# Kernel tuning notes

Measured on AMD Instinct MI355X. Metric: run time of the kernel, lower is better.

The kernel has to match this reference:

```python
import jax, jax.numpy as jnp
import numpy as np

N_NODES = 100000
N_EDGES = 3200000
F_IN = 128
F_OUT = 32
N_GRAPHS = 64


def setup_inputs() -> dict:
    key = jax.random.key(0)
    ks = jax.random.split(key, 12)
    x = jax.random.normal(ks[0], (N_NODES, F_IN), dtype=jnp.float32)
    edge_attr = jax.random.normal(ks[1], (N_EDGES, 1), dtype=jnp.float32)
    edge_index = jax.random.randint(ks[2], (2, N_EDGES), 0, N_NODES, dtype=jnp.int64)
    batch = jnp.sort(jax.random.randint(ks[3], (N_NODES,), 0, N_GRAPHS, dtype=jnp.int64))
    s = 1.0 / np.sqrt(F_IN)
    W_l = jax.random.normal(ks[4], (F_IN, F_OUT), dtype=jnp.float32) * s
    b_l = jnp.zeros((F_OUT,), dtype=jnp.float32)
    W_r = jax.random.normal(ks[5], (F_IN, F_OUT), dtype=jnp.float32) * s
    b_r = jnp.zeros((F_OUT,), dtype=jnp.float32)
    W_e = jax.random.normal(ks[6], (1, F_OUT), dtype=jnp.float32)
    att = jax.random.normal(ks[7], (F_OUT,), dtype=jnp.float32) * (1.0 / np.sqrt(F_OUT))
    bias = jnp.zeros((F_OUT,), dtype=jnp.float32)
    return {"x": x, "edge_attr": edge_attr, "W_l": W_l, "b_l": b_l,
            "W_r": W_r, "b_r": b_r, "W_e": W_e, "att": att, "bias": bias,
            "edge_index": edge_index, "batch": batch}


def reference(x, edge_attr, W_l, b_l, W_r, b_r, W_e, att, bias, edge_index, batch):
    # GATv2Conv (heads=1, concat=True, edge_dim=1, negative_slope=0.2)
    src = edge_index[0]  # message source j
    dst = edge_index[1]  # message target i
    xl = x @ W_l + b_l            # [N, F_OUT] source transform
    xr = x @ W_r + b_r            # [N, F_OUT] target transform
    e = edge_attr @ W_e           # [E, F_OUT] edge feature embedding
    m = xl[src] + xr[dst] + e     # [E, F_OUT]
    m = jax.nn.leaky_relu(m, negative_slope=0.2)
    logit = m @ att               # [E] per-edge attention logit
    # segment softmax over incoming edges of each target node
    mx = jax.ops.segment_max(logit, dst, num_segments=N_NODES)
    alpha = jnp.exp(logit - mx[dst])
    denom = jax.ops.segment_sum(alpha, dst, num_segments=N_NODES)
    alpha = alpha / (denom[dst] + 1e-16)
    # weighted scatter aggregation of source messages, then output bias
    out = jax.ops.segment_sum(xl[src] * alpha[:, None], dst, num_segments=N_NODES) + bias
    # global_mean_pool over graphs
    cnt = jax.ops.segment_sum(jnp.ones((N_NODES,), x.dtype), batch, num_segments=N_GRAPHS)
    pooled = jax.ops.segment_sum(out, batch, num_segments=N_GRAPHS) / jnp.maximum(cnt, 1.0)[:, None]
    return pooled  # [N_GRAPHS, F_OUT]
```

## Files before the change

kernel.cpp:

```cpp
#include <hip/hip_runtime.h>

#define N_NODES 100000
#define N_EDGES 3200000
#define F_IN 128
#define F_OUT 32
#define N_GRAPHS 64

__global__ __launch_bounds__(256) void gat_transform(
    const float* __restrict__ x,
    const float* __restrict__ Wl, const float* __restrict__ bl,
    const float* __restrict__ Wr, const float* __restrict__ br,
    float* __restrict__ xl, float* __restrict__ xr)
{
    __shared__ float sWl[F_IN * F_OUT];
    __shared__ float sWr[F_IN * F_OUT];
    for (int i = threadIdx.x; i < F_IN * F_OUT; i += 256) {
        sWl[i] = Wl[i];
        sWr[i] = Wr[i];
    }
    __syncthreads();

    const int f     = threadIdx.x & 31;
    const int local = threadIdx.x >> 5;
    const int node  = blockIdx.x * 8 + local;
    if (node >= N_NODES) return;

    const float4* xrow = (const float4*)(x + (size_t)node * F_IN);
    float accl = bl[f];
    float accr = br[f];
#pragma unroll
    for (int k4 = 0; k4 < F_IN / 4; ++k4) {
        float4 v = xrow[k4];
        const int k = k4 * 4;
        accl += v.x * sWl[(k + 0) * 32 + f];  accr += v.x * sWr[(k + 0) * 32 + f];
        accl += v.y * sWl[(k + 1) * 32 + f];  accr += v.y * sWr[(k + 1) * 32 + f];
        accl += v.z * sWl[(k + 2) * 32 + f];  accr += v.z * sWr[(k + 2) * 32 + f];
        accl += v.w * sWl[(k + 3) * 32 + f];  accr += v.w * sWr[(k + 3) * 32 + f];
    }
    xl[(size_t)node * 32 + f] = accl;
    xr[(size_t)node * 32 + f] = accr;
}

__global__ __launch_bounds__(256) void gat_edge(
    const int* __restrict__ ei,
    const float* __restrict__ eattr,
    const float* __restrict__ We,
    const float* __restrict__ att,
    const float* __restrict__ xl, const float* __restrict__ xr,
    float* __restrict__ outacc,
    float* __restrict__ denom)
{
    const int f = threadIdx.x & 31;
    const float attf = att[f];
    const float wef  = We[f];

    const int group   = (blockIdx.x * blockDim.x + threadIdx.x) >> 5;
    const int ngroups = (gridDim.x * blockDim.x) >> 5;

    for (int e = group; e < N_EDGES; e += ngroups) {
        const int src = ei[e];
        const int dst = ei[N_EDGES + e];
        const float ea = eattr[e];

        const float xlv = xl[(size_t)src * 32 + f];
        float m = xlv + xr[(size_t)dst * 32 + f] + ea * wef;
        m = (m > 0.f) ? m : 0.2f * m;

        float t = m * attf;
        t += __shfl_xor(t, 16, 32);
        t += __shfl_xor(t, 8, 32);
        t += __shfl_xor(t, 4, 32);
        t += __shfl_xor(t, 2, 32);
        t += __shfl_xor(t, 1, 32);

        const float p = __expf(t);
        atomicAdd(&outacc[(size_t)dst * 32 + f], xlv * p);
        if (f == 0) atomicAdd(&denom[dst], p);
    }
}

__global__ __launch_bounds__(256) void gat_pool(
    const float* __restrict__ outacc, const float* __restrict__ denom,
    const float* __restrict__ bias, const int* __restrict__ batch,
    float* __restrict__ out)
{
    const int g = blockIdx.x;
    __shared__ int s_lo, s_hi;
    if (threadIdx.x == 0) {
        int lo = 0, hi = N_NODES;
        while (lo < hi) { int mid = (lo + hi) >> 1; if (batch[mid] < g) lo = mid + 1; else hi = mid; }
        s_lo = lo;
        lo = 0; hi = N_NODES;
        while (lo < hi) { int mid = (lo + hi) >> 1; if (batch[mid] < g + 1) lo = mid + 1; else hi = mid; }
        s_hi = lo;
    }
    __syncthreads();
    const int lo = s_lo, hi = s_hi;

    const int f   = threadIdx.x & 31;
    const int grp = threadIdx.x >> 5;

    float acc = 0.f;
    for (int n = lo + grp; n < hi; n += 8) {
        const float d = denom[n];
        acc += outacc[(size_t)n * 32 + f] / (d + 1e-16f);
    }

    __shared__ float s_acc[8][32];
    s_acc[grp][f] = acc;
    __syncthreads();

    if (threadIdx.x < 32) {
        float sum = 0.f;
#pragma unroll
        for (int i = 0; i < 8; ++i) sum += s_acc[i][f];
        const int cnt = hi - lo;
        out[g * 32 + f] = (cnt > 0) ? (sum / (float)cnt + bias[f]) : 0.f;
    }
}

extern "C" void kernel_launch(void* const* d_in, const int* in_sizes, int n_in,
                              void* d_out, int out_size, void* d_ws, size_t ws_size,
                              hipStream_t stream)
{
    const float* x     = (const float*)d_in[0];
    const float* eattr = (const float*)d_in[1];
    const float* Wl    = (const float*)d_in[2];
    const float* bl    = (const float*)d_in[3];
    const float* Wr    = (const float*)d_in[4];
    const float* br    = (const float*)d_in[5];
    const float* We    = (const float*)d_in[6];
    const float* att   = (const float*)d_in[7];
    const float* bias  = (const float*)d_in[8];
    const int*   ei    = (const int*)d_in[9];
    const int*   batch = (const int*)d_in[10];
    float* out = (float*)d_out;

    float* ws = (float*)d_ws;
    float* xl     = ws;
    float* xr     = ws + (size_t)N_NODES * 32;
    float* outacc = ws + (size_t)N_NODES * 64;
    float* denom  = ws + (size_t)N_NODES * 96;

    hipMemsetAsync(outacc, 0, (size_t)N_NODES * 33 * sizeof(float), stream);

    gat_transform<<<(N_NODES + 7) / 8, 256, 0, stream>>>(x, Wl, bl, Wr, br, xl, xr);
    gat_edge<<<4096, 256, 0, stream>>>(ei, eattr, We, att, xl, xr, outacc, denom);
    gat_pool<<<N_GRAPHS, 256, 0, stream>>>(outacc, denom, bias, batch, out);
}
```

Before: 623.9 us.

## Build CSR by destination each call and aggregate per node without atomics

Replaces the per-edge atomic scatter with an on-device CSR build (degree histogram, two-level scan, atomic-offset scatter of src and edge_attr pairs). A per-node wavefront then gathers its incoming edges and keeps accumulator and denominator in registers. The normalized result is written in place over xr, which removes the float atomics into a 100000x32 buffer and the division in the pool kernel. The trade is several extra passes over the edge list plus integer atomics in the histogram and scatter steps, and per-node loops that are imbalanced when degrees vary. If the workspace is too small it falls back to the old atomic path.

```diff
diff --git a/kernel.cpp b/kernel.cpp
--- a/kernel.cpp
+++ b/kernel.cpp
@@ -5,6 +5,9 @@
 #define F_IN 128
 #define F_OUT 32
 #define N_GRAPHS 64
+
+#define SCAN_CHUNK 512
+#define N_CHUNKS ((N_NODES + SCAN_CHUNK - 1) / SCAN_CHUNK)
 
 __global__ __launch_bounds__(256) void gat_transform(
     const float* __restrict__ x,
@@ -41,48 +44,130 @@
     xr[(size_t)node * 32 + f] = accr;
 }
 
-__global__ __launch_bounds__(256) void gat_edge(
-    const int* __restrict__ ei,
-    const float* __restrict__ eattr,
-    const float* __restrict__ We,
-    const float* __restrict__ att,
-    const float* __restrict__ xl, const float* __restrict__ xr,
-    float* __restrict__ outacc,
-    float* __restrict__ denom)
-{
-    const int f = threadIdx.x & 31;
+__global__ __launch_bounds__(256) void csr_hist(const int* __restrict__ ei,
+                                                int* __restrict__ deg)
+{
+    const int stride = gridDim.x * blockDim.x;
+    for (int e = blockIdx.x * blockDim.x + threadIdx.x; e < N_EDGES; e += stride)
+        atomicAdd(&deg[ei[N_EDGES + e]], 1);
+}
+
+__global__ __launch_bounds__(256) void csr_scan_partial(const int* __restrict__ deg,
+                                                        int* __restrict__ partial)
+{
+    __shared__ int s[256];
+    const int c = blockIdx.x;
+    int v = 0;
+#pragma unroll
+    for (int r = 0; r < SCAN_CHUNK / 256; ++r) {
+        const int i = c * SCAN_CHUNK + r * 256 + threadIdx.x;
+        if (i < N_NODES) v += deg[i];
+    }
+    s[threadIdx.x] = v;
+    __syncthreads();
+    for (int off = 128; off > 0; off >>= 1) {
+        if (threadIdx.x < off) s[threadIdx.x] += s[threadIdx.x + off];
+        __syncthreads();
+    }
+    if (threadIdx.x == 0) partial[c] = s[0];
+}
+
+__global__ __launch_bounds__(256) void csr_scan_base(const int* __restrict__ partial,
+                                                     int* __restrict__ cbase)
+{
+    __shared__ int s[256];
+    const int t = threadIdx.x;
+    const int v = (t < N_CHUNKS) ? partial[t] : 0;
+    s[t] = v;
+    __syncthreads();
+    for (int off = 1; off < 256; off <<= 1) {
+        int u = (t >= off) ? s[t - off] : 0;
+        __syncthreads();
+        s[t] += u;
+        __syncthreads();
+    }
+    if (t < N_CHUNKS) cbase[t] = s[t] - v;
+}
+
+__global__ __launch_bounds__(256) void csr_scan_write(const int* __restrict__ deg,
+                                                      const int* __restrict__ cbase,
+                                                      int* __restrict__ rowptr,
+                                                      int* __restrict__ wofs)
+{
+    __shared__ int s[256];
+    const int c = blockIdx.x, t = threadIdx.x;
+    const int i0 = c * SCAN_CHUNK + 2 * t;
+    const int i1 = i0 + 1;
+    const int v0 = (i0 < N_NODES) ? deg[i0] : 0;
+    const int v1 = (i1 < N_NODES) ? deg[i1] : 0;
+    const int pv = v0 + v1;
+    s[t] = pv;
+    __syncthreads();
+    for (int off = 1; off < 256; off <<= 1) {
+        int u = (t >= off) ? s[t - off] : 0;
+        __syncthreads();
+        s[t] += u;
+        __syncthreads();
+    }
+    const int excl = s[t] - pv + cbase[c];
+    if (i0 < N_NODES) { rowptr[i0] = excl;      wofs[i0] = excl; }
+    if (i1 < N_NODES) { rowptr[i1] = excl + v0; wofs[i1] = excl + v0; }
+    if (c == 0 && t == 0) rowptr[N_NODES] = N_EDGES;
+}
+
+__global__ __launch_bounds__(256) void csr_scatter(const int* __restrict__ ei,
+                                                   const float* __restrict__ eattr,
+                                                   int* __restrict__ wofs,
+                                                   int2* __restrict__ es2)
+{
+    const int stride = gridDim.x * blockDim.x;
+    for (int e = blockIdx.x * blockDim.x + threadIdx.x; e < N_EDGES; e += stride) {
+        const int src = ei[e];
+        const int dst = ei[N_EDGES + e];
+        const int pos = atomicAdd(&wofs[dst], 1);
+        es2[pos] = make_int2(src, __float_as_int(eattr[e]));
+    }
+}
+
+__global__ __launch_bounds__(256) void gat_aggregate(
+    const int2* __restrict__ es2, const int* __restrict__ rowptr,
+    const float* __restrict__ We, const float* __restrict__ att,
+    const float* __restrict__ xl, float* xrh)
+{
+    const int f    = threadIdx.x & 31;
+    const int node = blockIdx.x * 8 + (threadIdx.x >> 5);
+    if (node >= N_NODES) return;
+
     const float attf = att[f];
     const float wef  = We[f];
-
-    const int group   = (blockIdx.x * blockDim.x + threadIdx.x) >> 5;
-    const int ngroups = (gridDim.x * blockDim.x) >> 5;
-
-    for (int e = group; e < N_EDGES; e += ngroups) {
-        const int src = ei[e];
-        const int dst = ei[N_EDGES + e];
-        const float ea = eattr[e];
-
+    const float xrf  = xrh[(size_t)node * 32 + f];
+    const int beg = rowptr[node];
+    const int end = rowptr[node + 1];
+
+    float acc = 0.f, den = 0.f;
+    for (int j = beg; j < end; ++j) {
+        const int2 pe = es2[j];
+        const int   src = pe.x;
+        const float ea  = __int_as_float(pe.y);
         const float xlv = xl[(size_t)src * 32 + f];
-        float m = xlv + xr[(size_t)dst * 32 + f] + ea * wef;
+        float m = xlv + xrf + ea * wef;
         m = (m > 0.f) ? m : 0.2f * m;
-
         float t = m * attf;
         t += __shfl_xor(t, 16, 32);
         t += __shfl_xor(t, 8, 32);
         t += __shfl_xor(t, 4, 32);
         t += __shfl_xor(t, 2, 32);
         t += __shfl_xor(t, 1, 32);
-
         const float p = __expf(t);
-        atomicAdd(&outacc[(size_t)dst * 32 + f], xlv * p);
-        if (f == 0) atomicAdd(&denom[dst], p);
-    }
+        acc += xlv * p;
+        den += p;
+    }
+    xrh[(size_t)node * 32 + f] = acc / (den + 1e-16f);
 }
 
 __global__ __launch_bounds__(256) void gat_pool(
-    const float* __restrict__ outacc, const float* __restrict__ denom,
-    const float* __restrict__ bias, const int* __restrict__ batch,
-    float* __restrict__ out)
+    const float* __restrict__ h, const float* __restrict__ bias,
+    const int* __restrict__ batch, float* __restrict__ out)
 {
     const int g = blockIdx.x;
     __shared__ int s_lo, s_hi;
@@ -101,10 +186,8 @@
     const int grp = threadIdx.x >> 5;
 
     float acc = 0.f;
-    for (int n = lo + grp; n < hi; n += 8) {
-        const float d = denom[n];
-        acc += outacc[(size_t)n * 32 + f] / (d + 1e-16f);
-    }
+    for (int n = lo + grp; n < hi; n += 8)
+        acc += h[(size_t)n * 32 + f];
 
     __shared__ float s_acc[8][32];
     s_acc[grp][f] = acc;
@@ -115,7 +198,70 @@
 #pragma unroll
         for (int i = 0; i < 8; ++i) sum += s_acc[i][f];
         const int cnt = hi - lo;
-        out[g * 32 + f] = (cnt > 0) ? (sum / (float)cnt + bias[f]) : 0.f;
+        out[g * 32 + f] = (cnt > 0) ? (sum / (float)cnt + bias[f]) : bias[f];
+    }
+}
+
+__global__ __launch_bounds__(256) void gat_edge_atomic(
+    const int* __restrict__ ei, const float* __restrict__ eattr,
+    const float* __restrict__ We, const float* __restrict__ att,
+    const float* __restrict__ xl, const float* __restrict__ xr,
+    float* __restrict__ outacc, float* __restrict__ denom)
+{
+    const int f = threadIdx.x & 31;
+    const float attf = att[f];
+    const float wef  = We[f];
+    const int group   = (blockIdx.x * blockDim.x + threadIdx.x) >> 5;
+    const int ngroups = (gridDim.x * blockDim.x) >> 5;
+    for (int e = group; e < N_EDGES; e += ngroups) {
+        const int src = ei[e];
+        const int dst = ei[N_EDGES + e];
+        const float xlv = xl[(size_t)src * 32 + f];
+        float m = xlv + xr[(size_t)dst * 32 + f] + eattr[e] * wef;
+        m = (m > 0.f) ? m : 0.2f * m;
+        float t = m * attf;
+        t += __shfl_xor(t, 16, 32);
+        t += __shfl_xor(t, 8, 32);
+        t += __shfl_xor(t, 4, 32);
+        t += __shfl_xor(t, 2, 32);
+        t += __shfl_xor(t, 1, 32);
+        const float p = __expf(t);
+        atomicAdd(&outacc[(size_t)dst * 32 + f], xlv * p);
+        if (f == 0) atomicAdd(&denom[dst], p);
+    }
+}
+
+__global__ __launch_bounds__(256) void gat_pool_div(
+    const float* __restrict__ outacc, const float* __restrict__ denom,
+    const float* __restrict__ bias, const int* __restrict__ batch,
+    float* __restrict__ out)
+{
+    const int g = blockIdx.x;
+    __shared__ int s_lo, s_hi;
+    if (threadIdx.x == 0) {
+        int lo = 0, hi = N_NODES;
+        while (lo < hi) { int mid = (lo + hi) >> 1; if (batch[mid] < g) lo = mid + 1; else hi = mid; }
+        s_lo = lo;
+        lo = 0; hi = N_NODES;
+        while (lo < hi) { int mid = (lo + hi) >> 1; if (batch[mid] < g + 1) lo = mid + 1; else hi = mid; }
+        s_hi = lo;
+    }
+    __syncthreads();
+    const int lo = s_lo, hi = s_hi;
+    const int f   = threadIdx.x & 31;
+    const int grp = threadIdx.x >> 5;
+    float acc = 0.f;
+    for (int n = lo + grp; n < hi; n += 8)
+        acc += outacc[(size_t)n * 32 + f] / (denom[n] + 1e-16f);
+    __shared__ float s_acc[8][32];
+    s_acc[grp][f] = acc;
+    __syncthreads();
+    if (threadIdx.x < 32) {
+        float sum = 0.f;
+#pragma unroll
+        for (int i = 0; i < 8; ++i) sum += s_acc[i][f];
+        const int cnt = hi - lo;
+        out[g * 32 + f] = (cnt > 0) ? (sum / (float)cnt + bias[f]) : bias[f];
     }
 }
 
@@ -137,14 +283,41 @@
     float* out = (float*)d_out;
 
     float* ws = (float*)d_ws;
-    float* xl     = ws;
-    float* xr     = ws + (size_t)N_NODES * 32;
-    float* outacc = ws + (size_t)N_NODES * 64;
-    float* denom  = ws + (size_t)N_NODES * 96;
-
-    hipMemsetAsync(outacc, 0, (size_t)N_NODES * 33 * sizeof(float), stream);
-
-    gat_transform<<<(N_NODES + 7) / 8, 256, 0, stream>>>(x, Wl, bl, Wr, br, xl, xr);
-    gat_edge<<<4096, 256, 0, stream>>>(ei, eattr, We, att, xl, xr, outacc, denom);
-    gat_pool<<<N_GRAPHS, 256, 0, stream>>>(outacc, denom, bias, batch, out);
-}
+    const size_t NF = (size_t)N_NODES * 32;
+
+    const size_t need_csr = (NF * 2) * 4 + (size_t)N_EDGES * 8
+                          + ((size_t)N_NODES * 2 + 1 + 256) * 4;
+
+    if (ws_size >= need_csr) {
+        float* xl  = ws;
+        float* xrh = ws + NF;
+        int2*  es2 = (int2*)(ws + 2 * NF);
+        int*   deg    = (int*)(es2 + N_EDGES);
+        int*   rowptr = deg + N_NODES;
+        int*   wofs   = rowptr + N_NODES + 1;
+        int*   partial = wofs + N_NODES;
+        int*   cbase   = partial;
+        cbase = partial + 256;
+
+        hipMemsetAsync(deg, 0, N_NODES * sizeof(int), stream);
+
+        csr_hist<<<2048, 256, 0, stream>>>(ei, deg);
+        csr_scan_partial<<<N_CHUNKS, 256, 0, stream>>>(deg, partial);
+        csr_scan_base<<<1, 256, 0, stream>>>(partial, cbase);
+        csr_scan_write<<<N_CHUNKS, 256, 0, stream>>>(deg, cbase, rowptr, wofs);
+        csr_scatter<<<2048, 256, 0, stream>>>(ei, eattr, wofs, es2);
+
+        gat_transform<<<(N_NODES + 7) / 8, 256, 0, stream>>>(x, Wl, bl, Wr, br, xl, xrh);
+        gat_aggregate<<<(N_NODES + 7) / 8, 256, 0, stream>>>(es2, rowptr, We, att, xl, xrh);
+        gat_pool<<<N_GRAPHS, 256, 0, stream>>>(xrh, bias, batch, out);
+    } else {
+        float* xl     = ws;
+        float* xr     = ws + NF;
+        float* outacc = ws + 2 * NF;
+        float* denom  = ws + 3 * NF;
+        hipMemsetAsync(outacc, 0, (NF + N_NODES) * sizeof(float), stream);
+        gat_transform<<<(N_NODES + 7) / 8, 256, 0, stream>>>(x, Wl, bl, Wr, br, xl, xr);
+        gat_edge_atomic<<<4096, 256, 0, stream>>>(ei, eattr, We, att, xl, xr, outacc, denom);
+        gat_pool_div<<<N_GRAPHS, 256, 0, stream>>>(outacc, denom, bias, batch, out);
+    }
+}
```

Result: slower. 711.0 us (+14.0%).

## Bucket edges by destination and aggregate per-bucket in shared memory

Applied to the files above, without the earlier changes.

Replaces the global-atomic edge kernel with a counting-sort of edges into destination buckets of 49 nodes (histogram, scan, scatter with packed src/local-dst/attr), then a per-bucket kernel that keeps xr, accumulators and denominators in shared memory and writes normalized outputs. This removes global float atomics on 3.2M×32 features and the separate normalization read in pooling. It adds two extra passes over the edge list plus a scatter with global atomics on counters. Weights are also interleaved as float2 in the transform kernel.

```diff
diff --git a/kernel.cpp b/kernel.cpp
--- a/kernel.cpp
+++ b/kernel.cpp
@@ -6,23 +6,25 @@
 #define F_OUT 32
 #define N_GRAPHS 64
 
+#define NB 2048
+#define BN 49
+#define NSLICE 8
+#define NCNT (NB * NSLICE)
+#define HGRID 2048
+
 __global__ __launch_bounds__(256) void gat_transform(
     const float* __restrict__ x,
     const float* __restrict__ Wl, const float* __restrict__ bl,
     const float* __restrict__ Wr, const float* __restrict__ br,
     float* __restrict__ xl, float* __restrict__ xr)
 {
-    __shared__ float sWl[F_IN * F_OUT];
-    __shared__ float sWr[F_IN * F_OUT];
-    for (int i = threadIdx.x; i < F_IN * F_OUT; i += 256) {
-        sWl[i] = Wl[i];
-        sWr[i] = Wr[i];
-    }
-    __syncthreads();
-
-    const int f     = threadIdx.x & 31;
-    const int local = threadIdx.x >> 5;
-    const int node  = blockIdx.x * 8 + local;
+    __shared__ float2 sW[F_IN * F_OUT];
+    for (int i = threadIdx.x; i < F_IN * F_OUT; i += 256)
+        sW[i] = make_float2(Wl[i], Wr[i]);
+    __syncthreads();
+
+    const int f    = threadIdx.x & 31;
+    const int node = blockIdx.x * 8 + (threadIdx.x >> 5);
     if (node >= N_NODES) return;
 
     const float4* xrow = (const float4*)(x + (size_t)node * F_IN);
@@ -32,57 +34,148 @@
     for (int k4 = 0; k4 < F_IN / 4; ++k4) {
         float4 v = xrow[k4];
         const int k = k4 * 4;
-        accl += v.x * sWl[(k + 0) * 32 + f];  accr += v.x * sWr[(k + 0) * 32 + f];
-        accl += v.y * sWl[(k + 1) * 32 + f];  accr += v.y * sWr[(k + 1) * 32 + f];
-        accl += v.z * sWl[(k + 2) * 32 + f];  accr += v.z * sWr[(k + 2) * 32 + f];
-        accl += v.w * sWl[(k + 3) * 32 + f];  accr += v.w * sWr[(k + 3) * 32 + f];
+        float2 w0 = sW[(k + 0) * 32 + f]; accl += v.x * w0.x; accr += v.x * w0.y;
+        float2 w1 = sW[(k + 1) * 32 + f]; accl += v.y * w1.x; accr += v.y * w1.y;
+        float2 w2 = sW[(k + 2) * 32 + f]; accl += v.z * w2.x; accr += v.z * w2.y;
+        float2 w3 = sW[(k + 3) * 32 + f]; accl += v.w * w3.x; accr += v.w * w3.y;
     }
     xl[(size_t)node * 32 + f] = accl;
     xr[(size_t)node * 32 + f] = accr;
 }
 
-__global__ __launch_bounds__(256) void gat_edge(
-    const int* __restrict__ ei,
-    const float* __restrict__ eattr,
-    const float* __restrict__ We,
-    const float* __restrict__ att,
-    const float* __restrict__ xl, const float* __restrict__ xr,
-    float* __restrict__ outacc,
-    float* __restrict__ denom)
-{
-    const int f = threadIdx.x & 31;
+__global__ __launch_bounds__(256) void bkt_hist(const int* __restrict__ ei,
+                                                int* __restrict__ cnt)
+{
+    const int slice  = blockIdx.x & (NSLICE - 1);
+    const int stride = gridDim.x * blockDim.x;
+    for (int e = blockIdx.x * blockDim.x + threadIdx.x; e < N_EDGES; e += stride) {
+        const int dst = ei[N_EDGES + e];
+        atomicAdd(&cnt[(dst / BN) * NSLICE + slice], 1);
+    }
+}
+
+__global__ __launch_bounds__(256) void bkt_scan(const int* __restrict__ cnt,
+                                                int* __restrict__ base,
+                                                int* __restrict__ cursor)
+{
+    __shared__ int s[256];
+    const int t = threadIdx.x;
+    const int R = NCNT / 256;
+    int sum = 0;
+    for (int r = 0; r < R; ++r) sum += cnt[t * R + r];
+    s[t] = sum;
+    __syncthreads();
+    for (int off = 1; off < 256; off <<= 1) {
+        int u = (t >= off) ? s[t - off] : 0;
+        __syncthreads();
+        s[t] += u;
+        __syncthreads();
+    }
+    int run = s[t] - sum;
+    for (int r = 0; r < R; ++r) {
+        const int i = t * R + r;
+        const int c = cnt[i];
+        base[i] = run;
+        cursor[i] = run;
+        run += c;
+    }
+    if (t == 255) base[NCNT] = run;
+}
+
+__global__ __launch_bounds__(256) void bkt_scatter(const int* __restrict__ ei,
+                                                   const float* __restrict__ eattr,
+                                                   int* __restrict__ cursor,
+                                                   int2* __restrict__ es2)
+{
+    const int slice  = blockIdx.x & (NSLICE - 1);
+    const int stride = gridDim.x * blockDim.x;
+    for (int e = blockIdx.x * blockDim.x + threadIdx.x; e < N_EDGES; e += stride) {
+        const int src = ei[e];
+        const int dst = ei[N_EDGES + e];
+        const int b   = dst / BN;
+        const int dl  = dst - b * BN;
+        const int pos = atomicAdd(&cursor[b * NSLICE + slice], 1);
+        es2[pos] = make_int2(src | (dl << 17), __float_as_int(eattr[e]));
+    }
+}
+
+#define PROCESS(e, xv) do {                                                   \
+    const int dl_ = (e).x >> 17;                                              \
+    float m_ = (xv) + sxr[dl_ * 32 + f] + __int_as_float((e).y) * wef;        \
+    m_ = (m_ > 0.f) ? m_ : 0.2f * m_;                                         \
+    float t_ = m_ * attf;                                                     \
+    t_ += __shfl_xor(t_, 16, 32);                                             \
+    t_ += __shfl_xor(t_, 8, 32);                                              \
+    t_ += __shfl_xor(t_, 4, 32);                                              \
+    t_ += __shfl_xor(t_, 2, 32);                                              \
+    t_ += __shfl_xor(t_, 1, 32);                                              \
+    const float p_ = __expf(t_);                                              \
+    atomicAdd(&sacc[dl_ * 32 + f], (xv) * p_);                                \
+    if (f == 0) atomicAdd(&sden[dl_], p_);                                    \
+} while (0)
+
+__global__ __launch_bounds__(256) void gat_aggregate(
+    const int2* __restrict__ es2, const int* __restrict__ base,
+    const float* __restrict__ We, const float* __restrict__ att,
+    const float* __restrict__ xl, float* xrh)
+{
+    __shared__ float sxr[BN * 32];
+    __shared__ float sacc[BN * 32];
+    __shared__ float sden[BN];
+
+    const int b    = blockIdx.x;
+    const int n0   = b * BN;
+    const int n1   = (n0 + BN < N_NODES) ? (n0 + BN) : N_NODES;
+    const int nrow = n1 - n0;
+    const int tid  = threadIdx.x;
+
+    if (nrow > 0) {
+        for (int i = tid; i < nrow * 32; i += 256) {
+            sxr[i]  = xrh[(size_t)n0 * 32 + i];
+            sacc[i] = 0.f;
+        }
+        for (int i = tid; i < nrow; i += 256) sden[i] = 0.f;
+    }
+    __syncthreads();
+    if (nrow <= 0) return;
+
+    const int f = tid & 31;
+    const int g = tid >> 5;
     const float attf = att[f];
     const float wef  = We[f];
 
-    const int group   = (blockIdx.x * blockDim.x + threadIdx.x) >> 5;
-    const int ngroups = (gridDim.x * blockDim.x) >> 5;
-
-    for (int e = group; e < N_EDGES; e += ngroups) {
-        const int src = ei[e];
-        const int dst = ei[N_EDGES + e];
-        const float ea = eattr[e];
-
-        const float xlv = xl[(size_t)src * 32 + f];
-        float m = xlv + xr[(size_t)dst * 32 + f] + ea * wef;
-        m = (m > 0.f) ? m : 0.2f * m;
-
-        float t = m * attf;
-        t += __shfl_xor(t, 16, 32);
-        t += __shfl_xor(t, 8, 32);
-        t += __shfl_xor(t, 4, 32);
-        t += __shfl_xor(t, 2, 32);
-        t += __shfl_xor(t, 1, 32);
-
-        const float p = __expf(t);
-        atomicAdd(&outacc[(size_t)dst * 32 + f], xlv * p);
-        if (f == 0) atomicAdd(&denom[dst], p);
-    }
+    const int beg = base[b * NSLICE];
+    const int end = base[(b + 1) * NSLICE];
+
+    int j0 = beg;
+    for (; j0 + 32 <= end; j0 += 32) {
+        int2 e0 = es2[j0 + g];
+        int2 e1 = es2[j0 + g + 8];
+        int2 e2 = es2[j0 + g + 16];
+        int2 e3 = es2[j0 + g + 24];
+        float x0 = xl[(size_t)(e0.x & 0x1FFFF) * 32 + f];
+        float x1 = xl[(size_t)(e1.x & 0x1FFFF) * 32 + f];
+        float x2 = xl[(size_t)(e2.x & 0x1FFFF) * 32 + f];
+        float x3 = xl[(size_t)(e3.x & 0x1FFFF) * 32 + f];
+        PROCESS(e0, x0);
+        PROCESS(e1, x1);
+        PROCESS(e2, x2);
+        PROCESS(e3, x3);
+    }
+    for (int j = j0 + g; j < end; j += 8) {
+        int2 e = es2[j];
+        float xv = xl[(size_t)(e.x & 0x1FFFF) * 32 + f];
+        PROCESS(e, xv);
+    }
+    __syncthreads();
+
+    for (int i = tid; i < nrow * 32; i += 256)
+        xrh[(size_t)n0 * 32 + i] = sacc[i] / (sden[i >> 5] + 1e-16f);
 }
 
 __global__ __launch_bounds__(256) void gat_pool(
-    const float* __restrict__ outacc, const float* __restrict__ denom,
-    const float* __restrict__ bias, const int* __restrict__ batch,
-    float* __restrict__ out)
+    const float* __restrict__ h, const float* __restrict__ bias,
+    const int* __restrict__ batch, float* __restrict__ out)
 {
     const int g = blockIdx.x;
     __shared__ int s_lo, s_hi;
@@ -101,10 +194,8 @@
     const int grp = threadIdx.x >> 5;
 
     float acc = 0.f;
-    for (int n = lo + grp; n < hi; n += 8) {
-        const float d = denom[n];
-        acc += outacc[(size_t)n * 32 + f] / (d + 1e-16f);
-    }
+    for (int n = lo + grp; n < hi; n += 8)
+        acc += h[(size_t)n * 32 + f];
 
     __shared__ float s_acc[8][32];
     s_acc[grp][f] = acc;
@@ -137,14 +228,22 @@
     float* out = (float*)d_out;
 
     float* ws = (float*)d_ws;
+    const size_t NF = (size_t)N_NODES * 32;
+
     float* xl     = ws;
-    float* xr     = ws + (size_t)N_NODES * 32;
-    float* outacc = ws + (size_t)N_NODES * 64;
-    float* denom  = ws + (size_t)N_NODES * 96;
-
-    hipMemsetAsync(outacc, 0, (size_t)N_NODES * 33 * sizeof(float), stream);
-
-    gat_transform<<<(N_NODES + 7) / 8, 256, 0, stream>>>(x, Wl, bl, Wr, br, xl, xr);
-    gat_edge<<<4096, 256, 0, stream>>>(ei, eattr, We, att, xl, xr, outacc, denom);
-    gat_pool<<<N_GRAPHS, 256, 0, stream>>>(outacc, denom, bias, batch, out);
-}
+    float* xrh    = ws + NF;
+    int2*  es2    = (int2*)(ws + 2 * NF);
+    int*   cnt    = (int*)(es2 + N_EDGES);
+    int*   base   = cnt + NCNT;
+    int*   cursor = base + NCNT + 1;
+
+    hipMemsetAsync(cnt, 0, NCNT * sizeof(int), stream);
+
+    bkt_hist<<<HGRID, 256, 0, stream>>>(ei, cnt);
+    bkt_scan<<<1, 256, 0, stream>>>(cnt, base, cursor);
+    bkt_scatter<<<HGRID, 256, 0, stream>>>(ei, eattr, cursor, es2);
+
+    gat_transform<<<(N_NODES + 7) / 8, 256, 0, stream>>>(x, Wl, bl, Wr, br, xl, xrh);
+    gat_aggregate<<<NB, 256, 0, stream>>>(es2, base, We, att, xl, xrh);
+    gat_pool<<<N_GRAPHS, 256, 0, stream>>>(xrh, bias, batch, out);
+}
```

After: 1.083 ms. 1.74x slower.
